# Kernel tuning notes

Hardware: AMD Instinct MI355X
Metric: run time of the kernel (lower is better)

## Reference

```python
import jax, jax.numpy as jnp
import numpy as np


def setup_inputs() -> dict:
    key = jax.random.key(0)
    ks = jax.random.split(key, 5)
    d_out, d_in = 4096, 4096
    r = min(d_out, d_in)
    B, T = 4, 2048
    x = jax.random.normal(ks[0], (B, T, d_in), dtype=jnp.float32)
    U = jax.random.normal(ks[1], (d_out, r), dtype=jnp.float32)
    S = jax.random.uniform(ks[2], (r,), dtype=jnp.float32)
    Vt = jax.random.normal(ks[3], (r, d_in), dtype=jnp.float32)
    epsilon = jnp.zeros((r,), dtype=jnp.float32)
    bias = jax.random.normal(ks[4], (d_out,), dtype=jnp.float32)
    return {"x": x, "U": U, "S": S, "Vt": Vt, "epsilon": epsilon, "bias": bias}


def reference(x, U, S, Vt, epsilon, bias):
    # w = U @ diag(S + epsilon) @ Vt  (diag folded as column scale of U)
    w = (U * (S + epsilon)[None, :]) @ Vt  # [d_out, d_in]
    # F.linear: y = x @ w.T + bias
    return jnp.einsum('btk,ok->bto', x, w) + bias
```

## Files before the change

kernel.cpp:

```cpp
#include <hip/hip_runtime.h>
#include <hip/hip_bf16.h>
#include <stdint.h>

typedef __attribute__((ext_vector_type(4))) float f32x4;
typedef __attribute__((ext_vector_type(8))) short short8v;

typedef __attribute__((address_space(1))) void gvoid;
typedef __attribute__((address_space(3))) void lvoid;

#define GLD16(gp, lp) __builtin_amdgcn_global_load_lds((const gvoid*)(gp), (lvoid*)(lp), 16, 0, 0)

__device__ __forceinline__ unsigned short f2bf(float f) {
    union { float ff; unsigned uu; } a; a.ff = f;
    unsigned u = a.uu;
    u += 0x7FFFu + ((u >> 16) & 1u);
    return (unsigned short)(u >> 16);
}

__global__ __launch_bounds__(256) void prep_fused_kernel(
    const float* __restrict__ U, const float* __restrict__ S,
    const float* __restrict__ eps, unsigned short* __restrict__ Ub,
    const float* __restrict__ Vt, unsigned short* __restrict__ VtT) {
    __shared__ float tile[64][65];
    if (blockIdx.x < 8192) {
        long idx = ((long)blockIdx.x * 256 + threadIdx.x) * 8;
        int r = (int)(idx & 4095);
        f32x4 u0 = *(const f32x4*)(U + idx);
        f32x4 u1 = *(const f32x4*)(U + idx + 4);
        f32x4 s0 = *(const f32x4*)(S + r);
        f32x4 s1 = *(const f32x4*)(S + r + 4);
        f32x4 e0 = *(const f32x4*)(eps + r);
        f32x4 e1 = *(const f32x4*)(eps + r + 4);
        union { uint4 v; unsigned short s[8]; } o;
#pragma unroll
        for (int j = 0; j < 4; ++j) {
            o.s[j]     = f2bf(u0[j] * (s0[j] + e0[j]));
            o.s[j + 4] = f2bf(u1[j] * (s1[j] + e1[j]));
        }
        *(uint4*)(Ub + idx) = o.v;
    } else {
        int t  = blockIdx.x - 8192;
        int k0 = (t & 63) << 6;
        int r0 = (t >> 6) << 6;
        int tx = threadIdx.x & 63;
        int tq = threadIdx.x >> 6;
#pragma unroll
        for (int i = 0; i < 16; ++i) {
            int row = (i << 2) + tq;
            tile[row][tx] = Vt[(long)(r0 + row) * 4096 + k0 + tx];
        }
        __syncthreads();
#pragma unroll
        for (int i = 0; i < 16; ++i) {
            int krow = (i << 2) + tq;
            VtT[(long)(k0 + krow) * 4096 + r0 + tx] = f2bf(tile[tx][krow]);
        }
    }
}

__global__ __launch_bounds__(256) void cvt_bf16_kernel(
    const float* __restrict__ src, unsigned short* __restrict__ dst) {
    long idx = ((long)blockIdx.x * 256 + threadIdx.x) * 8;
    f32x4 v0 = *(const f32x4*)(src + idx);
    f32x4 v1 = *(const f32x4*)(src + idx + 4);
    union { uint4 v; unsigned short s[8]; } o;
#pragma unroll
    for (int j = 0; j < 4; ++j) {
        o.s[j]     = f2bf(v0[j]);
        o.s[j + 4] = f2bf(v1[j]);
    }
    *(uint4*)(dst + idx) = o.v;
}

#define MM(a, b, c) __builtin_amdgcn_mfma_f32_16x16x32_bf16(a, b, c, 0, 0, 0)

#define ARG(r) (As + (r) * 8192)
#define BRG(r) (Bs + (r) * 8192)

#define STAGE_A(r, koff) GLD16(A + gAr + (koff), ARG(r) + wave * 512)
#define STAGE_B(r, koff) GLD16(B + gBr + (koff), BRG(r) + wave * 512)

#define LOAD_A(r) do { \
    const unsigned short* _p = ARG(r) + aBase; \
    _Pragma("unroll") \
    for (int _m = 0; _m < 4; ++_m) aR[_m] = *(const short8v*)(_p + _m * 512); } while (0)

#define READ_B(r) do { \
    const unsigned short* _p = BRG(r) + bBase; \
    _Pragma("unroll") \
    for (int _n = 0; _n < 4; ++_n) bR[_n] = *(const short8v*)(_p + _n * 512); } while (0)

#define MFMA16 do { \
    __builtin_amdgcn_s_setprio(1); \
    _Pragma("unroll") \
    for (int _m = 0; _m < 4; ++_m) { \
        acc[_m][0] = MM(aR[_m], bR[0], acc[_m][0]); \
        acc[_m][1] = MM(aR[_m], bR[1], acc[_m][1]); \
        acc[_m][2] = MM(aR[_m], bR[2], acc[_m][2]); \
        acc[_m][3] = MM(aR[_m], bR[3], acc[_m][3]); \
    } \
    __builtin_amdgcn_s_setprio(0); } while (0)

#define VM2 asm volatile("s_waitcnt vmcnt(2)" ::: "memory")
#define BAR __builtin_amdgcn_s_barrier()

#define PHASE(rd, st, sk) do { \
    LOAD_A(rd); READ_B(rd); \
    STAGE_A(st, sk); STAGE_B(st, sk); \
    MFMA16; \
    VM2; BAR; } while (0)

template<int OUT_BF16, int BIAS, int DO_CVT>
__global__ __launch_bounds__(1024, 4) void gemm256_kernel(
    const unsigned short* __restrict__ A,
    const unsigned short* __restrict__ B,
    void* __restrict__ Cv, const float* __restrict__ bias,
    const float* __restrict__ xsrc, unsigned short* __restrict__ xdst,
    int M, int N, int K) {
    __shared__ unsigned short As[4 * 8192];
    __shared__ unsigned short Bs[4 * 8192];

    const int tid  = threadIdx.x;
    const int wave = tid >> 6;
    const int lane = tid & 63;
    const int fr   = lane & 15;
    const int fq   = lane >> 4;

    const int nwg = gridDim.x;
    const int bid = blockIdx.x;
    const int cpx = nwg >> 3;
    const int wg  = (bid & 7) * cpx + (bid >> 3);
    const int nmt = M >> 8;
    const long n0 = (long)(2 * (wg / cpx) + (wg & 1)) << 8;
    const long m0 = (long)((wg >> 1) & (nmt - 1)) << 8;

    const int wwr = wave >> 2;
    const int wwc = wave & 3;

    const int  rS  = tid >> 2;
    const int  sS  = (tid & 3) ^ ((rS >> 1) & 3);
    const long gAr = (m0 + rS) * K + sS * 8;
    const long gBr = (n0 + rS) * K + sS * 8;

    const int swz   = (fq ^ ((fr >> 1) & 3)) * 8;
    const int aBase = (wwr * 64 + fr) * 32 + swz;
    const int bBase = (wwc * 64 + fr) * 32 + swz;

    f32x4  acc[4][4] = {};
    short8v aR[4], bR[4];

    f32x4 xv;
    unsigned long long xaddr = 0;
    unsigned short* xs = nullptr;
    if constexpr (DO_CVT) {
        long base = (long)bid * 4096 + (long)tid * 4;
        xaddr = (unsigned long long)(uintptr_t)(xsrc + base);
        xs = xdst + base;
    }

    STAGE_A(0, 0);  STAGE_B(0, 0);
    STAGE_A(1, 32); STAGE_B(1, 32);
    STAGE_A(2, 64); STAGE_B(2, 64);
    VM2;
    BAR;

    const int nIter = K >> 7;
    for (int i = 0; i < nIter; ++i) {
        const int kA = 128 * i + 96;
        int k0n = 128 * i + 128; if (k0n >= K) k0n -= K;
        int k1n = 128 * i + 160; if (k1n >= K) k1n -= K;
        int k2n = 128 * i + 192; if (k2n >= K) k2n -= K;

        if constexpr (DO_CVT) {
            LOAD_A(0); READ_B(0);
            if (i) {
                union { unsigned uu[2]; unsigned short s[4]; } o;
#pragma unroll
                for (int j = 0; j < 4; ++j) o.s[j] = f2bf(xv[j]);
                *(uint2*)xs = *(uint2*)o.uu;
                xs += 1048576;
            }
            asm volatile("global_load_dwordx4 %0, %1, off"
                         : "=v"(xv) : "v"(xaddr));
            xaddr += 4194304ull;
            STAGE_A(3, kA); STAGE_B(3, kA);
            MFMA16;
            VM2; BAR;
        } else {
            PHASE(0, 3, kA);
        }
        PHASE(1, 0, k0n);
        PHASE(2, 1, k1n);
        PHASE(3, 2, k2n);
    }

    if constexpr (DO_CVT) {
        union { unsigned uu[2]; unsigned short s[4]; } o;
#pragma unroll
        for (int j = 0; j < 4; ++j) o.s[j] = f2bf(xv[j]);
        *(uint2*)xs = *(uint2*)o.uu;
    }

#pragma unroll
    for (int nf = 0; nf < 4; ++nf) {
        const int col = (int)n0 + wwc * 64 + nf * 16 + fr;
        float bv = BIAS ? bias[col] : 0.0f;
#pragma unroll
        for (int mf = 0; mf < 4; ++mf) {
            f32x4 v = acc[mf][nf];
            long rowb = m0 + wwr * 64 + mf * 16 + fq * 4;
#pragma unroll
            for (int j = 0; j < 4; ++j) {
                float val = v[j] + bv;
                long off = (rowb + j) * N + col;
                if (OUT_BF16) ((unsigned short*)Cv)[off] = f2bf(val);
                else          ((float*)Cv)[off] = val;
            }
        }
    }
}

extern "C" void kernel_launch(void* const* d_in, const int* in_sizes, int n_in,
                              void* d_out, int out_size, void* d_ws, size_t ws_size,
                              hipStream_t stream) {
    const float* x    = (const float*)d_in[0];
    const float* U    = (const float*)d_in[1];
    const float* S    = (const float*)d_in[2];
    const float* Vt   = (const float*)d_in[3];
    const float* eps  = (const float*)d_in[4];
    const float* bias = (const float*)d_in[5];
    float* out = (float*)d_out;

    char* ws = (char*)d_ws;
    unsigned short* Ub  = (unsigned short*)(ws);
    unsigned short* VtT = (unsigned short*)(ws + (size_t)(32 << 20));
    unsigned short* Wb  = (unsigned short*)(ws + (size_t)(64 << 20));

    prep_fused_kernel<<<12288, 256, 0, stream>>>(U, S, eps, Ub, Vt, VtT);

    if (ws_size >= ((size_t)160 << 20)) {
        unsigned short* Xb = (unsigned short*)(ws + ((size_t)96 << 20));
        gemm256_kernel<1, 0, 1><<<256, 1024, 0, stream>>>(
            Ub, VtT, (void*)Wb, nullptr, x, Xb, 4096, 4096, 4096);
        gemm256_kernel<0, 1, 0><<<512, 1024, 0, stream>>>(
            Xb, Wb, (void*)out, bias, nullptr, nullptr, 8192, 4096, 4096);
    } else {
        unsigned short* Xb = (unsigned short*)(ws);
        gemm256_kernel<1, 0, 0><<<256, 1024, 0, stream>>>(
            Ub, VtT, (void*)Wb, nullptr, nullptr, nullptr, 4096, 4096, 4096);
        cvt_bf16_kernel<<<16384, 256, 0, stream>>>(x, Xb);
        gemm256_kernel<0, 1, 0><<<512, 1024, 0, stream>>>(
            Xb, Wb, (void*)out, bias, nullptr, nullptr, 8192, 4096, 4096);
    }
}
```

Before: 459.5 us.

## Load A fragments directly from global into registers, halve threads per block

Measured after the change: 921.6 us. +100.6%, slower.

```diff
diff --git a/kernel.cpp b/kernel.cpp
--- a/kernel.cpp
+++ b/kernel.cpp
@@ -74,50 +74,59 @@
 
 #define MM(a, b, c) __builtin_amdgcn_mfma_f32_16x16x32_bf16(a, b, c, 0, 0, 0)
 
-#define ARG(r) (As + (r) * 8192)
 #define BRG(r) (Bs + (r) * 8192)
 
-#define STAGE_A(r, koff) GLD16(A + gAr + (koff), ARG(r) + wave * 512)
-#define STAGE_B(r, koff) GLD16(B + gBr + (koff), BRG(r) + wave * 512)
-
-#define LOAD_A(r) do { \
-    const unsigned short* _p = ARG(r) + aBase; \
-    _Pragma("unroll") \
-    for (int _m = 0; _m < 4; ++_m) aR[_m] = *(const short8v*)(_p + _m * 512); } while (0)
-
-#define READ_B(r) do { \
-    const unsigned short* _p = BRG(r) + bBase; \
-    _Pragma("unroll") \
-    for (int _n = 0; _n < 4; ++_n) bR[_n] = *(const short8v*)(_p + _n * 512); } while (0)
-
-#define MFMA16 do { \
+#define STAGE_B(r, koff) do { \
+    const unsigned short* _s = B + gBr + (koff); \
+    unsigned short* _d = BRG(r) + wave * 512; \
+    GLD16(_s, _d); GLD16(_s + (long)128 * K, _d + 4096); } while (0)
+
+#define LOAD_A_G(bk, kk) do { \
+    const unsigned short* _b = A + aGbase + (kk); \
+    _Pragma("unroll") \
+    for (int _h = 0; _h < 2; ++_h) \
+    _Pragma("unroll") \
+    for (int _m = 0; _m < 4; ++_m) \
+        aR[bk][_h][_m] = *(const short8v*)(_b + (long)(_h * 64 + _m * 16) * K); \
+} while (0)
+
+#define READ_B4(rd) do { \
+    const unsigned short* _p = BRG(rd) + bBase; \
+    _Pragma("unroll") \
+    for (int _n = 0; _n < 4; ++_n) bR[_n] = *(const short8v*)(_p + _n * 512); \
+} while (0)
+
+#define MFMA32(bk) do { \
     __builtin_amdgcn_s_setprio(1); \
     _Pragma("unroll") \
+    for (int _h = 0; _h < 2; ++_h) \
+    _Pragma("unroll") \
     for (int _m = 0; _m < 4; ++_m) { \
-        acc[_m][0] = MM(aR[_m], bR[0], acc[_m][0]); \
-        acc[_m][1] = MM(aR[_m], bR[1], acc[_m][1]); \
-        acc[_m][2] = MM(aR[_m], bR[2], acc[_m][2]); \
-        acc[_m][3] = MM(aR[_m], bR[3], acc[_m][3]); \
+        acc[_h*4+_m][0] = MM(aR[bk][_h][_m], bR[0], acc[_h*4+_m][0]); \
+        acc[_h*4+_m][1] = MM(aR[bk][_h][_m], bR[1], acc[_h*4+_m][1]); \
+        acc[_h*4+_m][2] = MM(aR[bk][_h][_m], bR[2], acc[_h*4+_m][2]); \
+        acc[_h*4+_m][3] = MM(aR[bk][_h][_m], bR[3], acc[_h*4+_m][3]); \
     } \
     __builtin_amdgcn_s_setprio(0); } while (0)
 
-#define VM2 asm volatile("s_waitcnt vmcnt(2)" ::: "memory")
+#define VMW(n) asm volatile("s_waitcnt vmcnt(" #n ")" ::: "memory")
 #define BAR __builtin_amdgcn_s_barrier()
 
-#define PHASE(rd, st, sk) do { \
-    LOAD_A(rd); READ_B(rd); \
-    STAGE_A(st, sk); STAGE_B(st, sk); \
-    MFMA16; \
-    VM2; BAR; } while (0)
+#define PHASE(rd, st, sk, lk, lb, cb) do { \
+    READ_B4(rd); \
+    LOAD_A_G(lb, lk); \
+    STAGE_B(st, sk); \
+    VMW(10); \
+    MFMA32(cb); \
+    BAR; } while (0)
 
 template<int OUT_BF16, int BIAS, int DO_CVT>
-__global__ __launch_bounds__(1024, 4) void gemm256_kernel(
+__global__ __launch_bounds__(512, 2) void gemm256_kernel(
     const unsigned short* __restrict__ A,
     const unsigned short* __restrict__ B,
     void* __restrict__ Cv, const float* __restrict__ bias,
     const float* __restrict__ xsrc, unsigned short* __restrict__ xdst,
     int M, int N, int K) {
-    __shared__ unsigned short As[4 * 8192];
     __shared__ unsigned short Bs[4 * 8192];
 
     const int tid  = threadIdx.x;
@@ -139,66 +148,74 @@
 
     const int  rS  = tid >> 2;
     const int  sS  = (tid & 3) ^ ((rS >> 1) & 3);
-    const long gAr = (m0 + rS) * K + sS * 8;
     const long gBr = (n0 + rS) * K + sS * 8;
 
     const int swz   = (fq ^ ((fr >> 1) & 3)) * 8;
-    const int aBase = (wwr * 64 + fr) * 32 + swz;
     const int bBase = (wwc * 64 + fr) * 32 + swz;
 
-    f32x4  acc[4][4] = {};
-    short8v aR[4], bR[4];
-
-    f32x4 xv;
-    unsigned long long xaddr = 0;
+    const long aGbase = (m0 + wwr * 128 + fr) * K + fq * 8;
+
+    f32x4  acc[8][4] = {};
+    short8v aR[2][2][4], bR[4];
+
+    f32x4 xv0, xv1;
+    const float* xp = nullptr;
     unsigned short* xs = nullptr;
     if constexpr (DO_CVT) {
-        long base = (long)bid * 4096 + (long)tid * 4;
-        xaddr = (unsigned long long)(uintptr_t)(xsrc + base);
+        long base = (long)bid * 4096 + (long)tid * 8;
+        xp = xsrc + base;
         xs = xdst + base;
     }
 
-    STAGE_A(0, 0);  STAGE_B(0, 0);
-    STAGE_A(1, 32); STAGE_B(1, 32);
-    STAGE_A(2, 64); STAGE_B(2, 64);
-    VM2;
+    STAGE_B(0, 0);
+    STAGE_B(1, 32);
+    LOAD_A_G(0, 0);
+    VMW(10);
     BAR;
 
     const int nIter = K >> 7;
     for (int i = 0; i < nIter; ++i) {
-        const int kA = 128 * i + 96;
-        int k0n = 128 * i + 128; if (k0n >= K) k0n -= K;
-        int k1n = 128 * i + 160; if (k1n >= K) k1n -= K;
-        int k2n = 128 * i + 192; if (k2n >= K) k2n -= K;
+        const int k2 = 128 * i + 64;
+        const int k3 = 128 * i + 96;
+        int k4 = 128 * i + 128; if (k4 >= K) k4 -= K;
+        int k5 = 128 * i + 160; if (k5 >= K) k5 -= K;
 
         if constexpr (DO_CVT) {
-            LOAD_A(0); READ_B(0);
+            READ_B4(0);
             if (i) {
-                union { unsigned uu[2]; unsigned short s[4]; } o;
-#pragma unroll
-                for (int j = 0; j < 4; ++j) o.s[j] = f2bf(xv[j]);
-                *(uint2*)xs = *(uint2*)o.uu;
+                union { uint4 v; unsigned short s[8]; } o;
+#pragma unroll
+                for (int j = 0; j < 4; ++j) {
+                    o.s[j]     = f2bf(xv0[j]);
+                    o.s[j + 4] = f2bf(xv1[j]);
+                }
+                *(uint4*)xs = o.v;
                 xs += 1048576;
             }
-            asm volatile("global_load_dwordx4 %0, %1, off"
-                         : "=v"(xv) : "v"(xaddr));
-            xaddr += 4194304ull;
-            STAGE_A(3, kA); STAGE_B(3, kA);
-            MFMA16;
-            VM2; BAR;
+            xv0 = *(const f32x4*)(xp);
+            xv1 = *(const f32x4*)(xp + 4);
+            xp += 1048576;
+            LOAD_A_G(1, 128 * i + 32);
+            STAGE_B(2, k2);
+            if (i) VMW(13); else VMW(12);
+            MFMA32(0);
+            BAR;
         } else {
-            PHASE(0, 3, kA);
-        }
-        PHASE(1, 0, k0n);
-        PHASE(2, 1, k1n);
-        PHASE(3, 2, k2n);
+            PHASE(0, 2, k2, 128 * i + 32, 1, 0);
+        }
+        PHASE(1, 3, k3, 128 * i + 64, 0, 1);
+        PHASE(2, 0, k4, 128 * i + 96, 1, 0);
+        PHASE(3, 1, k5, k4,            0, 1);
     }
 
     if constexpr (DO_CVT) {
-        union { unsigned uu[2]; unsigned short s[4]; } o;
-#pragma unroll
-        for (int j = 0; j < 4; ++j) o.s[j] = f2bf(xv[j]);
-        *(uint2*)xs = *(uint2*)o.uu;
+        union { uint4 v; unsigned short s[8]; } o;
+#pragma unroll
+        for (int j = 0; j < 4; ++j) {
+            o.s[j]     = f2bf(xv0[j]);
+            o.s[j + 4] = f2bf(xv1[j]);
+        }
+        *(uint4*)xs = o.v;
     }
 
 #pragma unroll
@@ -206,9 +223,9 @@
         const int col = (int)n0 + wwc * 64 + nf * 16 + fr;
         float bv = BIAS ? bias[col] : 0.0f;
 #pragma unroll
-        for (int mf = 0; mf < 4; ++mf) {
+        for (int mf = 0; mf < 8; ++mf) {
             f32x4 v = acc[mf][nf];
-            long rowb = m0 + wwr * 64 + mf * 16 + fq * 4;
+            long rowb = m0 + wwr * 128 + mf * 16 + fq * 4;
 #pragma unroll
             for (int j = 0; j < 4; ++j) {
                 float val = v[j] + bv;
@@ -240,16 +257,16 @@
 
     if (ws_size >= ((size_t)160 << 20)) {
         unsigned short* Xb = (unsigned short*)(ws + ((size_t)96 << 20));
-        gemm256_kernel<1, 0, 1><<<256, 1024, 0, stream>>>(
+        gemm256_kernel<1, 0, 1><<<256, 512, 0, stream>>>(
             Ub, VtT, (void*)Wb, nullptr, x, Xb, 4096, 4096, 4096);
-        gemm256_kernel<0, 1, 0><<<512, 1024, 0, stream>>>(
+        gemm256_kernel<0, 1, 0><<<512, 512, 0, stream>>>(
             Xb, Wb, (void*)out, bias, nullptr, nullptr, 8192, 4096, 4096);
     } else {
         unsigned short* Xb = (unsigned short*)(ws);
-        gemm256_kernel<1, 0, 0><<<256, 1024, 0, stream>>>(
+        gemm256_kernel<1, 0, 0><<<256, 512, 0, stream>>>(
             Ub, VtT, (void*)Wb, nullptr, nullptr, nullptr, 4096, 4096, 4096);
         cvt_bf16_kernel<<<16384, 256, 0, stream>>>(x, Xb);
-        gemm256_kernel<0, 1, 0><<<512, 1024, 0, stream>>>(
+        gemm256_kernel<0, 1, 0><<<512, 512, 0, stream>>>(
             Xb, Wb, (void*)out, bias, nullptr, nullptr, 8192, 4096, 4096);
     }
 }
```
